# Optimization experiments

Measured on AMD Instinct MI355X. Metric: run time of the kernel, lower is better.

## Reference

```python
import jax, jax.numpy as jnp
import numpy as np


def setup_inputs() -> dict:
    key = jax.random.key(0)
    ks = jax.random.split(key, 5)
    B, S, H, I, E = 4, 2048, 1024, 4096, 8
    scale_in = 1.0 / np.sqrt(H)
    scale_mid = 1.0 / np.sqrt(I)
    return {
        "x": jax.random.normal(ks[0], (B, S, H), dtype=jnp.float32),
        "w_gate": jax.random.normal(ks[1], (H, E), dtype=jnp.float32) * scale_in,
        "w1": jax.random.normal(ks[2], (E, H, I), dtype=jnp.float32) * scale_in,
        "w2": jax.random.normal(ks[3], (E, I, H), dtype=jnp.float32) * scale_mid,
        "w3": jax.random.normal(ks[4], (E, H, I), dtype=jnp.float32) * scale_in,
        "num_experts_per_tok": 2,
    }


def reference(x, w_gate, w1, w2, w3, num_experts_per_tok):
    """MoE with top-k routing and SwiGLU experts (Mixtral-style).

    x: [B, S, H]; w_gate: [H, E]; w1/w3: [E, H, I]; w2: [E, I, H].
    Returns [B, S, H]. Matches torch module output (aux_loss is a side
    attribute in the original, not returned).
    """
    B, S, H = x.shape
    E = w_gate.shape[1]
    K = num_experts_per_tok
    xf = x.reshape(-1, H)                           # [T, H]

    logits = xf @ w_gate                            # [T, E]
    probs = jax.nn.softmax(logits, axis=-1)
    topk_probs, topk_idx = jax.lax.top_k(probs, K)  # [T, K]
    topk_probs = topk_probs / topk_probs.sum(axis=-1, keepdims=True)

    # Per-token per-expert combine weight: sum over k of renormalized top-k
    # probs mapped back to expert slots. [T, E]
    comb = jnp.sum(jax.nn.one_hot(topk_idx, E, dtype=xf.dtype)
                   * topk_probs[..., None], axis=1)

    out = jnp.zeros_like(xf)
    for e in range(E):  # small fixed loop over experts
        hidden = jax.nn.silu(xf @ w1[e]) * (xf @ w3[e])  # [T, I]
        out = out + (hidden @ w2[e]) * comb[:, e:e + 1]
    return out.reshape(B, S, H)
```

## Files before the change

### kernel.cpp

```cpp
#include <hip/hip_runtime.h>

typedef unsigned short u16;
typedef __attribute__((ext_vector_type(4))) float f32x4;
typedef __attribute__((ext_vector_type(8))) short s16x8;

#define T_TOK 8192
#define HD    1024
#define ID    4096
#define NE    8
#define AK    (T_TOK * 2)
#define APAD  (AK + 256)
#define MTMAX 72

#define BAR()   __builtin_amdgcn_s_barrier()
#define SB0()   __builtin_amdgcn_sched_barrier(0)
#define PRIO1() __builtin_amdgcn_s_setprio(1)
#define PRIO0() __builtin_amdgcn_s_setprio(0)
#define WAITV6() asm volatile("s_waitcnt vmcnt(6)" ::: "memory")
#define WAITV8() asm volatile("s_waitcnt vmcnt(8)" ::: "memory")
#define LGKM0()  do { asm volatile("s_waitcnt lgkmcnt(0)" ::: "memory"); SB0(); } while (0)

__device__ __forceinline__ u16 f2bf(float f) {
  unsigned u = __builtin_bit_cast(unsigned, f);
  u += 0x7FFFu + ((u >> 16) & 1u);
  return (u16)(u >> 16);
}

__device__ __forceinline__ void gld16(u16* lds, const u16* g) {
  __builtin_amdgcn_global_load_lds(
      (const __attribute__((address_space(1))) unsigned int*)g,
      (__attribute__((address_space(3))) unsigned int*)lds, 16, 0, 0);
}


__global__ void k_init(int* counts) {
  if (threadIdx.x < NE) counts[threadIdx.x] = 0;
}

__global__ void k_offsets(const int* __restrict__ counts, int* offs, int* cursors,
                          int* __restrict__ tiles, int* __restrict__ ntile) {
  if (threadIdx.x == 0) {
    int s = 0;
    for (int e = 0; e < NE; ++e) { offs[e] = s; s += counts[e]; }
    offs[NE] = s;
    int nt = 0;
    for (int e = 0; e < NE; ++e)
      for (int m0 = 0; m0 < counts[e]; m0 += 256)
        tiles[nt++] = (e << 16) | (m0 >> 8);
    ntile[0] = nt;
    for (int i = nt; i < MTMAX; ++i) tiles[i] = 0;
  }
  if (threadIdx.x < NE) cursors[threadIdx.x] = 0;
}

__global__ __launch_bounds__(256) void k_scatter(
    const int* __restrict__ tidx, const int* __restrict__ offs,
    int* cursors, const float* __restrict__ tw,
    int* __restrict__ list, float* __restrict__ wlist) {
  int idx = blockIdx.x * 256 + threadIdx.x;
  if (idx >= AK) return;
  int e = tidx[idx];
  int p = atomicAdd(&cursors[e], 1);
  int a = offs[e] + p;
  list[a] = idx >> 1;
  wlist[a] = tw[idx];
}


#define NB_CVT 8192
#define NB_T13 16384
#define NB_T2  8192
#define NB_RTR 2048

__global__ __launch_bounds__(256) void k_prep(
    const float* __restrict__ x, const float* __restrict__ wg,
    const float* __restrict__ w1, const float* __restrict__ w2,
    const float* __restrict__ w3,
    u16* __restrict__ xb, u16* __restrict__ w13b, u16* __restrict__ w2b,
    int* __restrict__ tidx, float* __restrict__ tw, int* __restrict__ counts) {
  __shared__ char smem[32768];
  int bid = blockIdx.x, t = threadIdx.x;

  if (bid < NB_CVT) {
    int idx = bid * 256 + t;
    float4 v = ((const float4*)x)[idx];
    ushort4 o;
    o.x = f2bf(v.x); o.y = f2bf(v.y); o.z = f2bf(v.z); o.w = f2bf(v.w);
    ((ushort4*)xb)[idx] = o;
    return;
  }
  if (bid < NB_CVT + NB_T13) {
    u16 (*tile)[72] = (u16(*)[72])smem;
    int r = bid - NB_CVT;
    int bx = r & 63, by = (r >> 6) & 15, bz = r >> 10;
    int which = bz >> 3, e = bz & 7;
    const float* in = (which ? w3 : w1) + (size_t)e * HD * ID;
    int r0 = by * 64, c0 = bx * 64;
    int rr = t >> 4, cc = (t & 15) * 4;
#pragma unroll
    for (int i = 0; i < 4; ++i) {
      int rw = i * 16 + rr;
      float4 v = *(const float4*)&in[(size_t)(r0 + rw) * ID + c0 + cc];
      tile[cc + 0][rw] = f2bf(v.x);
      tile[cc + 1][rw] = f2bf(v.y);
      tile[cc + 2][rw] = f2bf(v.z);
      tile[cc + 3][rw] = f2bf(v.w);
    }
    __syncthreads();
    int c = t >> 3, ch = (t & 7) * 8;
#pragma unroll
    for (int j = 0; j < 2; ++j) {
      int crow = c0 + j * 32 + c;
      int pr = ((crow >> 4) << 5) + which * 16 + (crow & 15);
      *(s16x8*)&w13b[((size_t)e * 2 * ID + pr) * HD + r0 + ch] =
          *(const s16x8*)&tile[j * 32 + c][ch];
    }
    return;
  }
  if (bid < NB_CVT + NB_T13 + NB_T2) {
    u16 (*tile)[72] = (u16(*)[72])smem;
    int r = bid - NB_CVT - NB_T13;
    int bx = r & 15, by = (r >> 4) & 63, bz = r >> 10;
    const int R = ID, C = HD;
    size_t base = (size_t)bz * R * C;
    int r0 = by * 64, c0 = bx * 64;
    int rr = t >> 4, cc = (t & 15) * 4;
#pragma unroll
    for (int i = 0; i < 4; ++i) {
      int rw = i * 16 + rr;
      float4 v = *(const float4*)&w2[base + (size_t)(r0 + rw) * C + c0 + cc];
      tile[cc + 0][rw] = f2bf(v.x);
      tile[cc + 1][rw] = f2bf(v.y);
      tile[cc + 2][rw] = f2bf(v.z);
      tile[cc + 3][rw] = f2bf(v.w);
    }
    __syncthreads();
    int c = t >> 3, ch = (t & 7) * 8;
#pragma unroll
    for (int j = 0; j < 2; ++j) {
      int cr = j * 32 + c;
      *(s16x8*)&w2b[base + (size_t)(c0 + cr) * R + r0 + ch] =
          *(const s16x8*)&tile[cr][ch];
    }
    return;
  }
  {
    float* wgs = (float*)smem;
    int blockR = bid - NB_CVT - NB_T13 - NB_T2;
    for (int i = t; i < NE * HD; i += 256) {
      int h = i >> 3, e = i & 7;
      wgs[e * HD + h] = wg[i];
    }
    __syncthreads();
    int lane = t & 63, wid = t >> 6;
    int tok = blockR * 4 + wid;
    const float* xr = x + (size_t)tok * HD;
    double acc[NE];
#pragma unroll
    for (int e = 0; e < NE; ++e) acc[e] = 0.0;
    for (int i = 0; i < HD / 64; ++i) {
      float xv = xr[lane + i * 64];
#pragma unroll
      for (int e = 0; e < NE; ++e)
        acc[e] += (double)xv * (double)wgs[e * HD + lane + i * 64];
    }
#pragma unroll
    for (int e = 0; e < NE; ++e)
      for (int s = 32; s >= 1; s >>= 1) acc[e] += __shfl_xor(acc[e], s, 64);
    int e0 = 0; double m0 = acc[0];
    for (int e = 1; e < NE; ++e) if (acc[e] > m0) { m0 = acc[e]; e0 = e; }
    int e1 = -1; double m1 = -1e300;
    for (int e = 0; e < NE; ++e) if (e != e0 && acc[e] > m1) { m1 = acc[e]; e1 = e; }
    if (lane == 0) {
      double d = exp(m1 - m0);
      tidx[tok * 2] = e0; tidx[tok * 2 + 1] = e1;
      tw[tok * 2] = (float)(1.0 / (1.0 + d));
      tw[tok * 2 + 1] = (float)(d / (1.0 + d));
      atomicAdd(&counts[e0], 1);
      atomicAdd(&counts[e1], 1);
    }
  }
}


#define GEMM_CORE(NTK, NITER) \
  int wr = wid >> 2, wc = wid & 3; \
  int lane15 = lane & 15, lq = lane >> 4, sw8 = lane15 & 7; \
  f32x4 acc[8][4]; \
  _Pragma("unroll") for (int m = 0; m < 8; ++m) \
    _Pragma("unroll") for (int n = 0; n < 4; ++n) acc[m][n] = (f32x4){0.f,0.f,0.f,0.f}; \
  auto stgA = [&](int bb, int h, int kt) { \
    gld16(&As[bb][(h*128 + 0*64 + wid*8) * 64], gA[h*2+0] + kt*64); \
    gld16(&As[bb][(h*128 + 1*64 + wid*8) * 64], gA[h*2+1] + kt*64); }; \
  auto stgB = [&](int bb, int h, int kt) { \
    gld16(&Bs[bb][(h*128 + 0*64 + wid*8) * 64], gB[h*2+0] + kt*64); \
    gld16(&Bs[bb][(h*128 + 1*64 + wid*8) * 64], gB[h*2+1] + kt*64); }; \
  s16x8 a[4][2], b[4][2]; \
  auto rdA = [&](int bb, int mh) { \
    _Pragma("unroll") for (int mm = 0; mm < 4; ++mm) \
      _Pragma("unroll") for (int kk = 0; kk < 2; ++kk) \
        a[mm][kk] = *(const s16x8*)&As[bb][(mh*128 + wr*64 + mm*16 + lane15)*64 + (((kk*4+lq)^sw8)*8)]; }; \
  auto rdB = [&](int bb, int fh) { \
    _Pragma("unroll") for (int ff = 0; ff < 2; ++ff) \
      _Pragma("unroll") for (int kk = 0; kk < 2; ++kk) \
        b[fh*2+ff][kk] = *(const s16x8*)&Bs[bb][(fh*128 + wc*32 + ff*16 + lane15)*64 + (((kk*4+lq)^sw8)*8)]; }; \
  auto mf = [&](int mh, int fh) { \
    _Pragma("unroll") for (int mm = 0; mm < 4; ++mm) \
      _Pragma("unroll") for (int ff = 0; ff < 2; ++ff) { \
        acc[mh*4+mm][fh*2+ff] = __builtin_amdgcn_mfma_f32_16x16x32_bf16(a[mm][0], b[fh*2+ff][0], acc[mh*4+mm][fh*2+ff], 0, 0, 0); \
        acc[mh*4+mm][fh*2+ff] = __builtin_amdgcn_mfma_f32_16x16x32_bf16(a[mm][1], b[fh*2+ff][1], acc[mh*4+mm][fh*2+ff], 0, 0, 0); } }; \
   \
  stgA(0,0,0); stgB(0,0,0); stgA(0,1,0); stgB(0,1,0); stgA(1,0,1); stgB(1,0,1); \
  WAITV8(); BAR(); SB0(); \
  for (int i = 0; i < (NITER); ++i) { \
    int ku2 = (2*i+2) & ((NTK)-1), ku3 = (2*i+3) & ((NTK)-1); \
     rdA(0,0); rdB(0,0); stgA(1,1,2*i+1); WAITV6(); BAR(); LGKM0(); PRIO1(); mf(0,0); PRIO0(); BAR(); SB0(); \
     rdB(0,1); stgB(1,1,2*i+1); BAR(); LGKM0(); PRIO1(); mf(0,1); PRIO0(); BAR(); SB0(); \
     rdA(0,1); stgA(0,0,ku2); BAR(); LGKM0(); PRIO1(); mf(1,0); PRIO0(); BAR(); SB0(); \
     stgB(0,0,ku2); WAITV8(); BAR(); PRIO1(); mf(1,1); PRIO0(); BAR(); SB0(); \
     rdA(1,0); rdB(1,0); stgA(0,1,ku2); WAITV6(); BAR(); LGKM0(); PRIO1(); mf(0,0); PRIO0(); BAR(); SB0(); \
     rdB(1,1); stgB(0,1,ku2); BAR(); LGKM0(); PRIO1(); mf(0,1); PRIO0(); BAR(); SB0(); \
     rdA(1,1); stgA(1,0,ku3); BAR(); LGKM0(); PRIO1(); mf(1,0); PRIO0(); BAR(); SB0(); \
     stgB(1,0,ku3); WAITV8(); BAR(); PRIO1(); mf(1,1); PRIO0(); BAR(); SB0(); \
  }

__global__ __launch_bounds__(512, 1) void k_gemm1(
    const u16* __restrict__ xb, const u16* __restrict__ w13b,
    const int* __restrict__ list, const int* __restrict__ offs,
    const int* __restrict__ tiles, const int* __restrict__ ntile,
    u16* __restrict__ hidden) {
  int ti = blockIdx.y;
  if (ti >= ntile[0]) return;
  int packed = tiles[ti];
  int e = packed >> 16;
  int m0 = (packed & 0xFFFF) << 8;
  int aoff = offs[e];
  int cnt = offs[e + 1] - aoff;
  int n0 = blockIdx.x * 256;

  __shared__ u16 As[2][256 * 64];
  __shared__ u16 Bs[2][256 * 64];

  int tid = threadIdx.x, lane = tid & 63, wid = tid >> 6;
  int l8 = lane >> 3, c8 = lane & 7;
  int csrc = (c8 ^ l8) * 8;

  const u16* gA[4]; const u16* gB[4];
#pragma unroll
  for (int h = 0; h < 2; ++h)
#pragma unroll
    for (int c = 0; c < 2; ++c) {
      int row = h * 128 + c * 64 + wid * 8 + l8;
      int rr = m0 + row; if (rr > cnt - 1) rr = cnt - 1;
      gA[h*2+c] = xb + (size_t)list[aoff + rr] * HD + csrc;
      gB[h*2+c] = w13b + ((size_t)e * 2 * ID + n0 + row) * HD + csrc;
    }

  GEMM_CORE(HD / 64, HD / 128)

#pragma unroll
  for (int mh = 0; mh < 2; ++mh)
#pragma unroll
    for (int mm = 0; mm < 4; ++mm)
#pragma unroll
      for (int j = 0; j < 4; ++j) {
        int grow = m0 + mh * 128 + wr * 64 + mm * 16 + lq * 4 + j;
        if (grow < cnt) {
          size_t rbase = (size_t)(aoff + grow) * ID;
#pragma unroll
          for (int p = 0; p < 2; ++p) {
            float v1 = acc[mh*4+mm][2*p][j];
            float v3 = acc[mh*4+mm][2*p+1][j];
            float s = v1 / (1.0f + __expf(-v1));
            int icol = ((n0 + p * 128 + wc * 32) >> 1) + lane15;
            hidden[rbase + icol] = f2bf(s * v3);
          }
        }
      }
}

__global__ __launch_bounds__(512, 1) void k_gemm2(
    const u16* __restrict__ hidden, const u16* __restrict__ w2b,
    const int* __restrict__ offs, const int* __restrict__ list,
    const float* __restrict__ wlist, const int* __restrict__ tiles,
    const int* __restrict__ ntile, float* __restrict__ out) {
  int ti = blockIdx.y;
  if (ti >= ntile[0]) return;
  int packed = tiles[ti];
  int e = packed >> 16;
  int m0 = (packed & 0xFFFF) << 8;
  int aoff = offs[e];
  int cnt = offs[e + 1] - aoff;
  int n0 = (blockIdx.x & 3) * 256;
  int kc = (blockIdx.x >> 2) * 1024;

  __shared__ u16 As[2][256 * 64];
  __shared__ u16 Bs[2][256 * 64];

  int tid = threadIdx.x, lane = tid & 63, wid = tid >> 6;
  int l8 = lane >> 3, c8 = lane & 7;
  int csrc = (c8 ^ l8) * 8;

  const u16* gA[4]; const u16* gB[4];
#pragma unroll
  for (int h = 0; h < 2; ++h)
#pragma unroll
    for (int c = 0; c < 2; ++c) {
      int row = h * 128 + c * 64 + wid * 8 + l8;
      gA[h*2+c] = hidden + (size_t)(aoff + m0 + row) * ID + kc + csrc;
      gB[h*2+c] = w2b + ((size_t)e * HD + n0 + row) * ID + kc + csrc;
    }

  GEMM_CORE(1024 / 64, 1024 / 128)

#pragma unroll
  for (int mh = 0; mh < 2; ++mh)
#pragma unroll
    for (int mm = 0; mm < 4; ++mm)
#pragma unroll
      for (int j = 0; j < 4; ++j) {
        int grow = m0 + mh * 128 + wr * 64 + mm * 16 + lq * 4 + j;
        if (grow < cnt) {
          int a_ = aoff + grow;
          int tok = list[a_];
          float wgt = wlist[a_];
          float* orow = out + (size_t)tok * HD;
#pragma unroll
          for (int f = 0; f < 4; ++f) {
            int col = n0 + (f >> 1) * 128 + wc * 32 + (f & 1) * 16 + lane15;
            atomicAdd(&orow[col], wgt * acc[mh*4+mm][f][j]);
          }
        }
      }
}


extern "C" void kernel_launch(void* const* d_in, const int* in_sizes, int n_in,
                              void* d_out, int out_size, void* d_ws, size_t ws_size,
                              hipStream_t stream) {
  const float* x  = (const float*)d_in[0];
  const float* wg = (const float*)d_in[1];
  const float* w1 = (const float*)d_in[2];
  const float* w2 = (const float*)d_in[3];
  const float* w3 = (const float*)d_in[4];

  char* p = (char*)d_ws;
  auto alloc = [&](size_t bytes) {
    char* r = p;
    p += (bytes + 255) & ~(size_t)255;
    return r;
  };
  u16*   xb      = (u16*)alloc((size_t)T_TOK * HD * 2);
  u16*   w13b    = (u16*)alloc((size_t)NE * 2 * ID * HD * 2);
  u16*   w2b     = (u16*)alloc((size_t)NE * HD * ID * 2);
  u16*   hidden  = (u16*)alloc((size_t)APAD * ID * 2);
  int*   tidx    = (int*)alloc(AK * 4);
  float* tw      = (float*)alloc(AK * 4);
  int*   list    = (int*)alloc(AK * 4);
  float* wlist   = (float*)alloc(AK * 4);
  int*   counts  = (int*)alloc(64);
  int*   offs    = (int*)alloc(64);
  int*   cursors = (int*)alloc(64);
  int*   tiles   = (int*)alloc(MTMAX * 4);
  int*   ntile   = (int*)alloc(64);
  (void)ws_size; (void)in_sizes; (void)n_in;

  hipMemsetAsync(d_out, 0, (size_t)out_size * 4, stream);

  k_init<<<1, 64, 0, stream>>>(counts);
  k_prep<<<NB_CVT + NB_T13 + NB_T2 + NB_RTR, 256, 0, stream>>>(
      x, wg, w1, w2, w3, xb, w13b, w2b, tidx, tw, counts);
  k_offsets<<<1, 64, 0, stream>>>(counts, offs, cursors, tiles, ntile);
  k_scatter<<<AK / 256, 256, 0, stream>>>(tidx, offs, cursors, tw, list, wlist);

  dim3 gg1(2 * ID / 256, MTMAX, 1);
  k_gemm1<<<gg1, 512, 0, stream>>>(xb, w13b, list, offs, tiles, ntile, hidden);
  dim3 gg2(16, MTMAX, 1);
  k_gemm2<<<gg2, 512, 0, stream>>>(hidden, w2b, offs, list, wlist, tiles, ntile,
                                   (float*)d_out);
}
```

Baseline: 1.012 ms.

## Replace gemm2 float atomics with bf16 split-K partials and combine kernel

The second expert GEMM no longer does scattered float atomicAdds into the output. It writes per-split-K bf16 partial results indexed by assignment slot, reusing the w13b buffer for three of the four slices. A new combine kernel sums the four partials for each token's two expert slots, applies the routing weights, and writes the output. This also drops the output memset. In exchange it adds an extra write and read pass over the partials, plus a bf16 rounding of the partial sums.

```diff
diff --git a/kernel.cpp b/kernel.cpp
--- a/kernel.cpp
+++ b/kernel.cpp
@@ -24,6 +24,11 @@
   unsigned u = __builtin_bit_cast(unsigned, f);
   u += 0x7FFFu + ((u >> 16) & 1u);
   return (u16)(u >> 16);
+}
+
+__device__ __forceinline__ float bf2f(u16 v) {
+  unsigned u = (unsigned)v << 16;
+  return __builtin_bit_cast(float, u);
 }
 
 __device__ __forceinline__ void gld16(u16* lds, const u16* g) {
@@ -55,15 +60,14 @@
 
 __global__ __launch_bounds__(256) void k_scatter(
     const int* __restrict__ tidx, const int* __restrict__ offs,
-    int* cursors, const float* __restrict__ tw,
-    int* __restrict__ list, float* __restrict__ wlist) {
+    int* cursors, int* __restrict__ list, int* __restrict__ pos) {
   int idx = blockIdx.x * 256 + threadIdx.x;
   if (idx >= AK) return;
   int e = tidx[idx];
   int p = atomicAdd(&cursors[e], 1);
   int a = offs[e] + p;
   list[a] = idx >> 1;
-  wlist[a] = tw[idx];
+  pos[idx] = a;
 }
 
 
@@ -281,9 +285,9 @@
 
 __global__ __launch_bounds__(512, 1) void k_gemm2(
     const u16* __restrict__ hidden, const u16* __restrict__ w2b,
-    const int* __restrict__ offs, const int* __restrict__ list,
-    const float* __restrict__ wlist, const int* __restrict__ tiles,
-    const int* __restrict__ ntile, float* __restrict__ out) {
+    const int* __restrict__ offs, const int* __restrict__ tiles,
+    const int* __restrict__ ntile,
+    u16* __restrict__ yp0, u16* __restrict__ yp3) {
   int ti = blockIdx.y;
   if (ti >= ntile[0]) return;
   int packed = tiles[ti];
@@ -292,7 +296,8 @@
   int aoff = offs[e];
   int cnt = offs[e + 1] - aoff;
   int n0 = (blockIdx.x & 3) * 256;
-  int kc = (blockIdx.x >> 2) * 1024;
+  int kidx = blockIdx.x >> 2;
+  int kc = kidx * 1024;
 
   __shared__ u16 As[2][256 * 64];
   __shared__ u16 Bs[2][256 * 64];
@@ -313,6 +318,7 @@
 
   GEMM_CORE(1024 / 64, 1024 / 128)
 
+  u16* yp = (kidx < 3) ? yp0 + (size_t)kidx * AK * HD : yp3;
 #pragma unroll
   for (int mh = 0; mh < 2; ++mh)
 #pragma unroll
@@ -321,17 +327,39 @@
       for (int j = 0; j < 4; ++j) {
         int grow = m0 + mh * 128 + wr * 64 + mm * 16 + lq * 4 + j;
         if (grow < cnt) {
-          int a_ = aoff + grow;
-          int tok = list[a_];
-          float wgt = wlist[a_];
-          float* orow = out + (size_t)tok * HD;
+          u16* yrow = yp + (size_t)(aoff + grow) * HD;
 #pragma unroll
           for (int f = 0; f < 4; ++f) {
             int col = n0 + (f >> 1) * 128 + wc * 32 + (f & 1) * 16 + lane15;
-            atomicAdd(&orow[col], wgt * acc[mh*4+mm][f][j]);
+            yrow[col] = f2bf(acc[mh*4+mm][f][j]);
           }
         }
       }
+}
+
+__global__ __launch_bounds__(256) void k_combine(
+    const u16* __restrict__ yp0, const u16* __restrict__ yp3,
+    const int* __restrict__ pos, const float* __restrict__ tw,
+    float* __restrict__ out) {
+  int t = blockIdx.x;
+  int c = threadIdx.x * 4;
+  int a0 = pos[t * 2], a1 = pos[t * 2 + 1];
+  float w0 = tw[t * 2], w1 = tw[t * 2 + 1];
+  float s0[4] = {0.f, 0.f, 0.f, 0.f}, s1[4] = {0.f, 0.f, 0.f, 0.f};
+#pragma unroll
+  for (int k = 0; k < 4; ++k) {
+    const u16* yp = (k < 3) ? yp0 + (size_t)k * AK * HD : yp3;
+    ushort4 v0 = *(const ushort4*)&yp[(size_t)a0 * HD + c];
+    ushort4 v1 = *(const ushort4*)&yp[(size_t)a1 * HD + c];
+    s0[0] += bf2f(v0.x); s0[1] += bf2f(v0.y); s0[2] += bf2f(v0.z); s0[3] += bf2f(v0.w);
+    s1[0] += bf2f(v1.x); s1[1] += bf2f(v1.y); s1[2] += bf2f(v1.z); s1[3] += bf2f(v1.w);
+  }
+  float4 o;
+  o.x = w0 * s0[0] + w1 * s1[0];
+  o.y = w0 * s0[1] + w1 * s1[1];
+  o.z = w0 * s0[2] + w1 * s1[2];
+  o.w = w0 * s0[3] + w1 * s1[3];
+  *(float4*)&out[(size_t)t * HD + c] = o;
 }
 
 
@@ -354,28 +382,29 @@
   u16*   w13b    = (u16*)alloc((size_t)NE * 2 * ID * HD * 2);
   u16*   w2b     = (u16*)alloc((size_t)NE * HD * ID * 2);
   u16*   hidden  = (u16*)alloc((size_t)APAD * ID * 2);
+  u16*   yp3     = (u16*)alloc((size_t)AK * HD * 2);
   int*   tidx    = (int*)alloc(AK * 4);
   float* tw      = (float*)alloc(AK * 4);
   int*   list    = (int*)alloc(AK * 4);
-  float* wlist   = (float*)alloc(AK * 4);
+  int*   pos     = (int*)alloc(AK * 4);
   int*   counts  = (int*)alloc(64);
   int*   offs    = (int*)alloc(64);
   int*   cursors = (int*)alloc(64);
   int*   tiles   = (int*)alloc(MTMAX * 4);
   int*   ntile   = (int*)alloc(64);
-  (void)ws_size; (void)in_sizes; (void)n_in;
-
-  hipMemsetAsync(d_out, 0, (size_t)out_size * 4, stream);
+  (void)ws_size; (void)in_sizes; (void)n_in; (void)out_size;
+
+  u16* yp0 = w13b;
 
   k_init<<<1, 64, 0, stream>>>(counts);
   k_prep<<<NB_CVT + NB_T13 + NB_T2 + NB_RTR, 256, 0, stream>>>(
       x, wg, w1, w2, w3, xb, w13b, w2b, tidx, tw, counts);
   k_offsets<<<1, 64, 0, stream>>>(counts, offs, cursors, tiles, ntile);
-  k_scatter<<<AK / 256, 256, 0, stream>>>(tidx, offs, cursors, tw, list, wlist);
+  k_scatter<<<AK / 256, 256, 0, stream>>>(tidx, offs, cursors, list, pos);
 
   dim3 gg1(2 * ID / 256, MTMAX, 1);
   k_gemm1<<<gg1, 512, 0, stream>>>(xb, w13b, list, offs, tiles, ntile, hidden);
   dim3 gg2(16, MTMAX, 1);
-  k_gemm2<<<gg2, 512, 0, stream>>>(hidden, w2b, offs, list, wlist, tiles, ntile,
-                                   (float*)d_out);
-}
+  k_gemm2<<<gg2, 512, 0, stream>>>(hidden, w2b, offs, tiles, ntile, yp0, yp3);
+  k_combine<<<T_TOK, 256, 0, stream>>>(yp0, yp3, pos, tw, (float*)d_out);
+}
```

New measurement: 876.9 us. 1.15x faster.
